# Performance work log

Hardware: AMD Instinct MI355X
Metric: run time of the kernel (lower is better)

Reference implementation:

```python
import jax, jax.numpy as jnp
import numpy as np

NUM_PERTS = 20000
D = 256          # embedding_dim
B, C = 64, 512   # batch_size, num_cells
EPS = 1e-5


def setup_inputs() -> dict:
    key = jax.random.key(0)
    ks = jax.random.split(key, 20)
    inp = {
        'perturbation_ids': jax.random.randint(ks[0], (B, C), 0, NUM_PERTS),
        'table': jax.random.normal(ks[1], (NUM_PERTS, D), dtype=jnp.float32),
    }
    s = 1.0 / np.sqrt(D)
    for i in range(4):
        inp[f'W{i+1}'] = jax.random.uniform(ks[2 + 2 * i], (D, D), minval=-s, maxval=s, dtype=jnp.float32)
        inp[f'b{i+1}'] = jax.random.uniform(ks[3 + 2 * i], (D,), minval=-s, maxval=s, dtype=jnp.float32)
    for i in range(3):
        inp[f'g{i+1}'] = jnp.ones((D,), jnp.float32)
        inp[f'be{i+1}'] = jnp.zeros((D,), jnp.float32)
    return inp


def _bn(x, gamma, beta):
    # BatchNorm1d forward with batch statistics (training-mode math, biased var)
    mu = jnp.mean(x, axis=0)
    var = jnp.mean(jnp.square(x - mu), axis=0)
    return (x - mu) * jax.lax.rsqrt(var + EPS) * gamma + beta


def reference(perturbation_ids, table,
              W1, b1, W2, b2, W3, b3, W4, b4,
              g1, be1, g2, be2, g3, be3):
    # Vectorized replacement of the Python double-loop dict gather
    emb = table[perturbation_ids]                 # (B, C, D)
    x = emb.reshape(-1, D)                        # (B*C, D)
    x = _bn(jax.nn.gelu(x @ W1 + b1, approximate=False), g1, be1)
    x = _bn(jax.nn.gelu(x @ W2 + b2, approximate=False), g2, be2)
    x = _bn(jax.nn.gelu(x @ W3 + b3, approximate=False), g3, be3)
    x = jax.nn.gelu(x @ W4 + b4, approximate=False)
    return x.reshape(B, C, D)
```

## Files before the change

### kernel.cpp

```cpp
#include <hip/hip_runtime.h>
#include <math.h>


typedef __attribute__((ext_vector_type(8))) short short8;
typedef __attribute__((ext_vector_type(4))) float floatx4;

#define DDIM 256

__device__ __forceinline__ unsigned short f2bf(float f) {
    union { float f; unsigned int u; } v; v.f = f;
    unsigned int r = v.u + 0x7fffu + ((v.u >> 16) & 1u);
    return (unsigned short)(r >> 16);
}
__device__ __forceinline__ float gelu_fast(float x) {
    float z = 0.7978845608f * (x + 0.044715f * x * x * x);
    float e = __expf(2.0f * z);
    float th = 1.0f - 2.0f * __builtin_amdgcn_rcpf(1.0f + e);
    return 0.5f * x * (1.0f + th);
}

__global__ void prep_kernel(const float* __restrict__ W1,
                            unsigned short* __restrict__ W1t,
                            float* __restrict__ stats )
{
    const int t = threadIdx.x, b = blockIdx.x;
    W1t[(size_t)t * DDIM + b] = f2bf(W1[(size_t)b * DDIM + t]);
    if (b < 12) {
        float* s = stats + b * 1024;
        s[t] = 0.f; s[t + 256] = 0.f; s[t + 512] = 0.f; s[t + 768] = 0.f;
    }
}

template<int GATHER, int WRITE_F32, int DO_STATS>
__global__ __launch_bounds__(256, 2)
void gemm_enc(const unsigned short* __restrict__ A,
              const int* __restrict__ ids,
              const float* __restrict__ table,
              const unsigned short* __restrict__ Wt,
              const float* __restrict__ bias,
              void* __restrict__ outp,
              float* __restrict__ statShards )
{
    __shared__ alignas(16) unsigned short Albs[64 * 256];

    const int tid  = threadIdx.x;
    const int blk  = blockIdx.x;
    const int wave = tid >> 6;
    const int lane = tid & 63;
    const int quad = lane >> 4;
    const int l15  = lane & 15;
    const int wn   = wave;
    const int row0 = blk * 64;

    {
        const int r  = tid >> 2;
        const int c0 = (tid & 3) * 64;
        if (GATHER) {
            const int src = ids[row0 + r];
            const float* tp = table + (size_t)src * DDIM + c0;
#pragma unroll
            for (int j = 0; j < 8; ++j) {
                float4 v0 = *(const float4*)(tp + j * 8);
                float4 v1 = *(const float4*)(tp + j * 8 + 4);
                union { unsigned short u[8]; uint4 v; } o;
                o.u[0]=f2bf(v0.x); o.u[1]=f2bf(v0.y); o.u[2]=f2bf(v0.z); o.u[3]=f2bf(v0.w);
                o.u[4]=f2bf(v1.x); o.u[5]=f2bf(v1.y); o.u[6]=f2bf(v1.z); o.u[7]=f2bf(v1.w);
                const int g = (tid & 3) * 8 + j;
                *(uint4*)(Albs + r * 256 + (g ^ (r & 7)) * 8) = o.v;
            }
        } else {
            const unsigned short* ap = A + (size_t)(row0 + r) * DDIM + c0;
#pragma unroll
            for (int j = 0; j < 8; ++j) {
                uint4 v = *(const uint4*)(ap + j * 8);
                const int g = (tid & 3) * 8 + j;
                *(uint4*)(Albs + r * 256 + (g ^ (r & 7)) * 8) = v;
            }
        }
    }

    float bias_v[4];
#pragma unroll
    for (int nt = 0; nt < 4; ++nt)
        bias_v[nt] = bias[wn * 64 + nt * 16 + l15];

    floatx4 acc[4][4];
#pragma unroll
    for (int i = 0; i < 4; ++i)
#pragma unroll
        for (int j = 0; j < 4; ++j)
            acc[i][j] = floatx4{0.f, 0.f, 0.f, 0.f};

    __syncthreads();

    const unsigned short* wb = Wt + (size_t)(wn * 64 + l15) * DDIM + quad * 8;
#pragma unroll 2
    for (int kk = 0; kk < 8; ++kk) {
        short8 bfr[4];
#pragma unroll
        for (int nt = 0; nt < 4; ++nt)
            bfr[nt] = *(const short8*)(wb + (size_t)(nt * 16) * DDIM + kk * 32);
        short8 af[4];
        const int agp = ((kk * 4 + quad) ^ (l15 & 7)) * 8;
#pragma unroll
        for (int mt = 0; mt < 4; ++mt)
            af[mt] = *(const short8*)(Albs + (mt * 16 + l15) * 256 + agp);
#pragma unroll
        for (int mt = 0; mt < 4; ++mt)
#pragma unroll
            for (int nt = 0; nt < 4; ++nt)
                acc[mt][nt] = __builtin_amdgcn_mfma_f32_16x16x32_bf16(
                    af[mt], bfr[nt], acc[mt][nt], 0, 0, 0);
    }

    float s1[4] = {0.f, 0.f, 0.f, 0.f};
    float s2[4] = {0.f, 0.f, 0.f, 0.f};
#pragma unroll
    for (int mt = 0; mt < 4; ++mt) {
        const int rb = row0 + mt * 16 + quad * 4;
#pragma unroll
        for (int nt = 0; nt < 4; ++nt) {
            const int col = wn * 64 + nt * 16 + l15;
#pragma unroll
            for (int i = 0; i < 4; ++i) {
                float y = gelu_fast(acc[mt][nt][i] + bias_v[nt]);
                if (WRITE_F32) {
                    ((float*)outp)[(size_t)(rb + i) * DDIM + col] = y;
                } else {
                    ((unsigned short*)outp)[(size_t)(rb + i) * DDIM + col] = f2bf(y);
                }
                if (DO_STATS) { s1[nt] += y; s2[nt] += y * y; }
            }
        }
    }
    if (DO_STATS) {
#pragma unroll
        for (int nt = 0; nt < 4; ++nt) {
            s1[nt] += __shfl_xor(s1[nt], 16); s1[nt] += __shfl_xor(s1[nt], 32);
            s2[nt] += __shfl_xor(s2[nt], 16); s2[nt] += __shfl_xor(s2[nt], 32);
        }
        float* sb = statShards + (blk & 7) * 512;
        if (quad == 0) {
#pragma unroll
            for (int nt = 0; nt < 4; ++nt) {
                const int col = wn * 64 + nt * 16 + l15;
                atomicAdd(&sb[col],       s1[nt]);
                atomicAdd(&sb[256 + col], s2[nt]);
            }
        }
    }
}

__global__ void fold_kernel(const float* __restrict__ shards,
                            const float* __restrict__ g,
                            const float* __restrict__ be,
                            const float* __restrict__ W,
                            const float* __restrict__ b,
                            unsigned short* __restrict__ Wt,
                            float* __restrict__ bOut)
{
    __shared__ float sc[256], sh[256], red[4];
    const int t = threadIdx.x;
    const int n = blockIdx.x;
    float sum = 0.f, sq = 0.f;
#pragma unroll
    for (int s = 0; s < 8; ++s) {
        sum += shards[s * 512 + t];
        sq  += shards[s * 512 + 256 + t];
    }
    const float mu  = sum * (1.0f / 32768.0f);
    const float var = sq * (1.0f / 32768.0f) - mu * mu;
    const float scale = rsqrtf(var + 1e-5f) * g[t];
    sc[t] = scale;
    sh[t] = be[t] - mu * scale;
    __syncthreads();
    const float w = W[t * DDIM + n];
    Wt[n * DDIM + t] = f2bf(sc[t] * w);
    float pp = sh[t] * w;
#pragma unroll
    for (int o = 32; o; o >>= 1) pp += __shfl_down(pp, o);
    if ((t & 63) == 0) red[t >> 6] = pp;
    __syncthreads();
    if (t == 0) bOut[n] = b[n] + red[0] + red[1] + red[2] + red[3];
}

extern "C" void kernel_launch(void* const* d_in, const int* in_sizes, int n_in,
                              void* d_out, int out_size, void* d_ws, size_t ws_size,
                              hipStream_t stream)
{
    const int*   ids   = (const int*)  d_in[0];
    const float* table = (const float*)d_in[1];
    const float* W1 = (const float*)d_in[2];  const float* b1 = (const float*)d_in[3];
    const float* W2 = (const float*)d_in[4];  const float* b2 = (const float*)d_in[5];
    const float* W3 = (const float*)d_in[6];  const float* b3 = (const float*)d_in[7];
    const float* W4 = (const float*)d_in[8];  const float* b4 = (const float*)d_in[9];
    const float* g1 = (const float*)d_in[10]; const float* be1 = (const float*)d_in[11];
    const float* g2 = (const float*)d_in[12]; const float* be2 = (const float*)d_in[13];
    const float* g3 = (const float*)d_in[14]; const float* be3 = (const float*)d_in[15];

    unsigned char* ws = (unsigned char*)d_ws;
    unsigned short* W1t = (unsigned short*)ws;
    unsigned short* W2t = (unsigned short*)(ws + (size_t)131072);
    unsigned short* W3t = (unsigned short*)(ws + (size_t)262144);
    unsigned short* W4t = (unsigned short*)(ws + (size_t)393216);
    float* bb2   = (float*)(ws + (size_t)524288);
    float* bb3   = (float*)(ws + (size_t)525312);
    float* bb4   = (float*)(ws + (size_t)526336);
    float* stats = (float*)(ws + (size_t)527360);
    unsigned short* act1 = (unsigned short*)(ws + (size_t)1048576);
    unsigned short* act2 = (unsigned short*)(ws + (size_t)17825792);

    prep_kernel<<<256, 256, 0, stream>>>(W1, W1t, stats);

    gemm_enc<1, 0, 1><<<512, 256, 0, stream>>>(nullptr, ids, table, W1t, b1,
                                               act1, stats);
    fold_kernel<<<256, 256, 0, stream>>>(stats, g1, be1, W2, b2, W2t, bb2);

    gemm_enc<0, 0, 1><<<512, 256, 0, stream>>>(act1, nullptr, nullptr, W2t, bb2,
                                               act2, stats + 4096);
    fold_kernel<<<256, 256, 0, stream>>>(stats + 4096, g2, be2, W3, b3, W3t, bb3);

    gemm_enc<0, 0, 1><<<512, 256, 0, stream>>>(act2, nullptr, nullptr, W3t, bb3,
                                               act1, stats + 8192);
    fold_kernel<<<256, 256, 0, stream>>>(stats + 8192, g3, be3, W4, b4, W4t, bb4);

    gemm_enc<0, 1, 0><<<512, 256, 0, stream>>>(act1, nullptr, nullptr, W4t, bb4,
                                               (void*)d_out, nullptr);
}
```

Before: 182.2 us.

## Apply BatchNorm affine on loaded activations and drop fold kernels

Removes the three fold kernels that folded the BatchNorm scale and shift into the next layer's weights and bias. Each GEMM now reduces the stat shards itself and applies the per-column affine to the bf16 activations while staging them in shared memory. All four weight transposes move into one prep kernel. Row tiles shrink from 64 to 32 with launch bounds raised to 4 blocks per CU, so there are twice as many blocks. In exchange, every block repeats the stats reduction and does extra per-element convert and FMA work during the load, plus one more rounding step to bf16.

```diff
diff --git a/kernel.cpp b/kernel.cpp
--- a/kernel.cpp
+++ b/kernel.cpp
@@ -11,6 +11,10 @@
     union { float f; unsigned int u; } v; v.f = f;
     unsigned int r = v.u + 0x7fffu + ((v.u >> 16) & 1u);
     return (unsigned short)(r >> 16);
+}
+__device__ __forceinline__ float bf2f(unsigned short u) {
+    union { unsigned int i; float f; } v; v.i = ((unsigned int)u) << 16;
+    return v.f;
 }
 __device__ __forceinline__ float gelu_fast(float x) {
     float z = 0.7978845608f * (x + 0.044715f * x * x * x);
@@ -19,29 +23,38 @@
     return 0.5f * x * (1.0f + th);
 }
 
-__global__ void prep_kernel(const float* __restrict__ W1,
-                            unsigned short* __restrict__ W1t,
+__global__ void prep_kernel(const float* __restrict__ W0,
+                            const float* __restrict__ W1,
+                            const float* __restrict__ W2,
+                            const float* __restrict__ W3,
+                            unsigned short* __restrict__ Wt ,
                             float* __restrict__ stats )
 {
     const int t = threadIdx.x, b = blockIdx.x;
-    W1t[(size_t)t * DDIM + b] = f2bf(W1[(size_t)b * DDIM + t]);
+    const int j = b >> 8, n = b & 255;
+    const float* W = (j == 0) ? W0 : (j == 1) ? W1 : (j == 2) ? W2 : W3;
+    Wt[((size_t)j << 16) + (size_t)t * DDIM + n] = f2bf(W[(size_t)n * DDIM + t]);
     if (b < 12) {
         float* s = stats + b * 1024;
         s[t] = 0.f; s[t + 256] = 0.f; s[t + 512] = 0.f; s[t + 768] = 0.f;
     }
 }
 
-template<int GATHER, int WRITE_F32, int DO_STATS>
-__global__ __launch_bounds__(256, 2)
+template<int GATHER, int AFFINE, int WRITE_F32, int DO_STATS>
+__global__ __launch_bounds__(256, 4)
 void gemm_enc(const unsigned short* __restrict__ A,
               const int* __restrict__ ids,
               const float* __restrict__ table,
               const unsigned short* __restrict__ Wt,
               const float* __restrict__ bias,
+              const float* __restrict__ statsIn,
+              const float* __restrict__ gma,
+              const float* __restrict__ bta,
               void* __restrict__ outp,
-              float* __restrict__ statShards )
+              float* __restrict__ statShards)
 {
-    __shared__ alignas(16) unsigned short Albs[64 * 256];
+    __shared__ alignas(16) unsigned short Albs[32 * 256];
+    __shared__ float sc[256], sh[256];
 
     const int tid  = threadIdx.x;
     const int blk  = blockIdx.x;
@@ -50,31 +63,55 @@
     const int quad = lane >> 4;
     const int l15  = lane & 15;
     const int wn   = wave;
-    const int row0 = blk * 64;
+    const int row0 = blk * 32;
+
+    if (AFFINE) {
+        float sum = 0.f, sq = 0.f;
+#pragma unroll
+        for (int s = 0; s < 8; ++s) {
+            sum += statsIn[s * 512 + tid];
+            sq  += statsIn[s * 512 + 256 + tid];
+        }
+        const float mu  = sum * (1.f / 32768.f);
+        const float var = sq * (1.f / 32768.f) - mu * mu;
+        const float scl = rsqrtf(var + 1e-5f) * gma[tid];
+        sc[tid] = scl;
+        sh[tid] = bta[tid] - mu * scl;
+        __syncthreads();
+    }
 
     {
-        const int r  = tid >> 2;
-        const int c0 = (tid & 3) * 64;
+        const int r  = tid & 31;
+        const int ci = tid >> 5;
+        const int c0 = ci * 32;
         if (GATHER) {
             const int src = ids[row0 + r];
             const float* tp = table + (size_t)src * DDIM + c0;
 #pragma unroll
-            for (int j = 0; j < 8; ++j) {
+            for (int j = 0; j < 4; ++j) {
                 float4 v0 = *(const float4*)(tp + j * 8);
                 float4 v1 = *(const float4*)(tp + j * 8 + 4);
                 union { unsigned short u[8]; uint4 v; } o;
                 o.u[0]=f2bf(v0.x); o.u[1]=f2bf(v0.y); o.u[2]=f2bf(v0.z); o.u[3]=f2bf(v0.w);
                 o.u[4]=f2bf(v1.x); o.u[5]=f2bf(v1.y); o.u[6]=f2bf(v1.z); o.u[7]=f2bf(v1.w);
-                const int g = (tid & 3) * 8 + j;
+                const int g = ci * 4 + j;
                 *(uint4*)(Albs + r * 256 + (g ^ (r & 7)) * 8) = o.v;
             }
         } else {
             const unsigned short* ap = A + (size_t)(row0 + r) * DDIM + c0;
 #pragma unroll
-            for (int j = 0; j < 8; ++j) {
-                uint4 v = *(const uint4*)(ap + j * 8);
-                const int g = (tid & 3) * 8 + j;
-                *(uint4*)(Albs + r * 256 + (g ^ (r & 7)) * 8) = v;
+            for (int j = 0; j < 4; ++j) {
+                union { unsigned short u[8]; uint4 v; } o;
+                o.v = *(const uint4*)(ap + j * 8);
+                if (AFFINE) {
+#pragma unroll
+                    for (int e = 0; e < 8; ++e) {
+                        const int c = c0 + j * 8 + e;
+                        o.u[e] = f2bf(fmaf(bf2f(o.u[e]), sc[c], sh[c]));
+                    }
+                }
+                const int g = ci * 4 + j;
+                *(uint4*)(Albs + r * 256 + (g ^ (r & 7)) * 8) = o.v;
             }
         }
     }
@@ -84,9 +121,9 @@
     for (int nt = 0; nt < 4; ++nt)
         bias_v[nt] = bias[wn * 64 + nt * 16 + l15];
 
-    floatx4 acc[4][4];
-#pragma unroll
-    for (int i = 0; i < 4; ++i)
+    floatx4 acc[2][4];
+#pragma unroll
+    for (int i = 0; i < 2; ++i)
 #pragma unroll
         for (int j = 0; j < 4; ++j)
             acc[i][j] = floatx4{0.f, 0.f, 0.f, 0.f};
@@ -100,13 +137,13 @@
 #pragma unroll
         for (int nt = 0; nt < 4; ++nt)
             bfr[nt] = *(const short8*)(wb + (size_t)(nt * 16) * DDIM + kk * 32);
-        short8 af[4];
+        short8 af[2];
         const int agp = ((kk * 4 + quad) ^ (l15 & 7)) * 8;
 #pragma unroll
-        for (int mt = 0; mt < 4; ++mt)
+        for (int mt = 0; mt < 2; ++mt)
             af[mt] = *(const short8*)(Albs + (mt * 16 + l15) * 256 + agp);
 #pragma unroll
-        for (int mt = 0; mt < 4; ++mt)
+        for (int mt = 0; mt < 2; ++mt)
 #pragma unroll
             for (int nt = 0; nt < 4; ++nt)
                 acc[mt][nt] = __builtin_amdgcn_mfma_f32_16x16x32_bf16(
@@ -116,7 +153,7 @@
     float s1[4] = {0.f, 0.f, 0.f, 0.f};
     float s2[4] = {0.f, 0.f, 0.f, 0.f};
 #pragma unroll
-    for (int mt = 0; mt < 4; ++mt) {
+    for (int mt = 0; mt < 2; ++mt) {
         const int rb = row0 + mt * 16 + quad * 4;
 #pragma unroll
         for (int nt = 0; nt < 4; ++nt) {
@@ -149,39 +186,6 @@
             }
         }
     }
-}
-
-__global__ void fold_kernel(const float* __restrict__ shards,
-                            const float* __restrict__ g,
-                            const float* __restrict__ be,
-                            const float* __restrict__ W,
-                            const float* __restrict__ b,
-                            unsigned short* __restrict__ Wt,
-                            float* __restrict__ bOut)
-{
-    __shared__ float sc[256], sh[256], red[4];
-    const int t = threadIdx.x;
-    const int n = blockIdx.x;
-    float sum = 0.f, sq = 0.f;
-#pragma unroll
-    for (int s = 0; s < 8; ++s) {
-        sum += shards[s * 512 + t];
-        sq  += shards[s * 512 + 256 + t];
-    }
-    const float mu  = sum * (1.0f / 32768.0f);
-    const float var = sq * (1.0f / 32768.0f) - mu * mu;
-    const float scale = rsqrtf(var + 1e-5f) * g[t];
-    sc[t] = scale;
-    sh[t] = be[t] - mu * scale;
-    __syncthreads();
-    const float w = W[t * DDIM + n];
-    Wt[n * DDIM + t] = f2bf(sc[t] * w);
-    float pp = sh[t] * w;
-#pragma unroll
-    for (int o = 32; o; o >>= 1) pp += __shfl_down(pp, o);
-    if ((t & 63) == 0) red[t >> 6] = pp;
-    __syncthreads();
-    if (t == 0) bOut[n] = b[n] + red[0] + red[1] + red[2] + red[3];
 }
 
 extern "C" void kernel_launch(void* const* d_in, const int* in_sizes, int n_in,
@@ -199,31 +203,23 @@
     const float* g3 = (const float*)d_in[14]; const float* be3 = (const float*)d_in[15];
 
     unsigned char* ws = (unsigned char*)d_ws;
-    unsigned short* W1t = (unsigned short*)ws;
-    unsigned short* W2t = (unsigned short*)(ws + (size_t)131072);
-    unsigned short* W3t = (unsigned short*)(ws + (size_t)262144);
-    unsigned short* W4t = (unsigned short*)(ws + (size_t)393216);
-    float* bb2   = (float*)(ws + (size_t)524288);
-    float* bb3   = (float*)(ws + (size_t)525312);
-    float* bb4   = (float*)(ws + (size_t)526336);
-    float* stats = (float*)(ws + (size_t)527360);
+    unsigned short* Wt   = (unsigned short*)ws;
+    float* stats = (float*)(ws + (size_t)524288);
     unsigned short* act1 = (unsigned short*)(ws + (size_t)1048576);
     unsigned short* act2 = (unsigned short*)(ws + (size_t)17825792);
-
-    prep_kernel<<<256, 256, 0, stream>>>(W1, W1t, stats);
-
-    gemm_enc<1, 0, 1><<<512, 256, 0, stream>>>(nullptr, ids, table, W1t, b1,
-                                               act1, stats);
-    fold_kernel<<<256, 256, 0, stream>>>(stats, g1, be1, W2, b2, W2t, bb2);
-
-    gemm_enc<0, 0, 1><<<512, 256, 0, stream>>>(act1, nullptr, nullptr, W2t, bb2,
-                                               act2, stats + 4096);
-    fold_kernel<<<256, 256, 0, stream>>>(stats + 4096, g2, be2, W3, b3, W3t, bb3);
-
-    gemm_enc<0, 0, 1><<<512, 256, 0, stream>>>(act2, nullptr, nullptr, W3t, bb3,
-                                               act1, stats + 8192);
-    fold_kernel<<<256, 256, 0, stream>>>(stats + 8192, g3, be3, W4, b4, W4t, bb4);
-
-    gemm_enc<0, 1, 0><<<512, 256, 0, stream>>>(act1, nullptr, nullptr, W4t, bb4,
-                                               (void*)d_out, nullptr);
-}
+    unsigned short* Wt1 = Wt;
+    unsigned short* Wt2 = Wt + 65536;
+    unsigned short* Wt3 = Wt + 131072;
+    unsigned short* Wt4 = Wt + 196608;
+
+    prep_kernel<<<1024, 256, 0, stream>>>(W1, W2, W3, W4, Wt, stats);
+
+    gemm_enc<1, 0, 0, 1><<<1024, 256, 0, stream>>>(
+        nullptr, ids, table, Wt1, b1, nullptr, nullptr, nullptr, act1, stats);
+    gemm_enc<0, 1, 0, 1><<<1024, 256, 0, stream>>>(
+        act1, nullptr, nullptr, Wt2, b2, stats, g1, be1, act2, stats + 4096);
+    gemm_enc<0, 1, 0, 1><<<1024, 256, 0, stream>>>(
+        act2, nullptr, nullptr, Wt3, b3, stats + 4096, g2, be2, act1, stats + 8192);
+    gemm_enc<0, 1, 1, 0><<<1024, 256, 0, stream>>>(
+        act1, nullptr, nullptr, Wt4, b4, stats + 8192, g3, be3, (void*)d_out, nullptr);
+}
```

Result: slower. 199.1 us (+9.3%).
